# Kernel tuning notes

Measured on AMD Instinct MI355X. Metric: run time of the kernel, lower is better.

Reference implementation:

```python
import jax, jax.numpy as jnp
import numpy as np
from jax import lax

# Fixed Sobel kernels, OIHW layout: [2 out, 1 in, 3, 3]
_GX = np.array([[1, 0, -1], [2, 0, -2], [1, 0, -1]], dtype=np.float32)
_GY = np.array([[1, 2, 1], [0, 0, 0], [-1, -2, -1]], dtype=np.float32)
SOBEL_K = jnp.asarray(np.stack([_GX, _GY], 0)[:, None])  # [2,1,3,3]


def setup_inputs() -> dict:
    key = jax.random.key(0)
    x = jax.random.normal(key, (16, 1, 1024, 1024), dtype=jnp.float32)
    return {"x": x}


def reference(x):
    # Sobel conv, padding=1 (SAME): y [B,2,H,W]
    y = lax.conv_general_dilated(
        x, SOBEL_K, window_strides=(1, 1), padding=((1, 1), (1, 1)),
        dimension_numbers=("NCHW", "OIHW", "NCHW"))
    # sb_x: cross-correlation with [1,-1] along W -> s[:, :-1] - s[:, 1:], then drop last row
    s0 = jnp.sign(y[:, 0:1])                       # [B,1,H,W]
    y0 = (s0[..., :-1] - s0[..., 1:])[..., :-1, :]  # [B,1,H-1,W-1]
    # sb_y: cross-correlation with [1,-1]^T along H -> s[:-1] - s[1:], then drop last col
    s1 = jnp.sign(y[:, 1:2])                       # [B,1,H,W]
    y1 = (s1[..., :-1, :] - s1[..., 1:, :])[..., :-1]  # [B,1,H-1,W-1]
    return (y, y0, y1)
```

## Files before the change

### kernel.cpp

```cpp
#include <hip/hip_runtime.h>


__device__ __forceinline__ void load_raw(const float* __restrict__ xb, int r, int t,
                                         float4& L, float4& C, float4& R) {
    if ((unsigned)r < 1024u) {
        const float4* __restrict__ rp = (const float4*)(xb + (r << 10));
        L = rp[(t > 0) ? (t - 1) : 0];
        C = rp[t];
        R = rp[(t < 255) ? (t + 1) : 255];
    } else {
        L = C = R = make_float4(0.f, 0.f, 0.f, 0.f);
    }
}

__device__ __forceinline__ void cvt_row(float4 L, float4 C, float4 R, int t,
                                        double* __restrict__ o ) {
    float lw = (t > 0)   ? L.w : 0.f;
    float r0 = (t < 255) ? R.x : 0.f;
    float r1 = (t < 255) ? R.y : 0.f;
    o[0] = (double)lw;  o[1] = (double)C.x; o[2] = (double)C.y; o[3] = (double)C.z;
    o[4] = (double)C.w; o[5] = (double)r0;  o[6] = (double)r1;
}

__device__ __forceinline__ float fsign(double v) {
    return (v > 0.0) ? 1.0f : ((v < 0.0) ? -1.0f : 0.0f);
}

__global__ __launch_bounds__(256) void sobel_sign_kernel(const float* __restrict__ x,
                                                         float* __restrict__ out) {
    const int t  = threadIdx.x;
    const int b  = blockIdx.x >> 7;
    const int hg = blockIdx.x & 127;
    const int h0 = hg << 3;
    const int w0 = t << 2;

    const float* __restrict__ xb = x + ((size_t)b << 20);
    float* __restrict__ yb = out + ((size_t)b << 21);
    const size_t NP = (size_t)1023 * 1023;
    float* __restrict__ Y0 = out + 33554432u + (size_t)b * NP;
    float* __restrict__ Y1 = out + 50298896u + (size_t)b * NP;

    __shared__ float s0[1024];
    __shared__ float s1[1024];

    double r[3][7];
    float4 L, C, R;
    load_raw(xb, h0 - 1, t, L, C, R); cvt_row(L, C, R, t, r[0]);
    load_raw(xb, h0,     t, L, C, R); cvt_row(L, C, R, t, r[1]);
    load_raw(xb, h0 + 1, t, L, C, R);

    float psgy[4];

    #pragma unroll
    for (int it = 0; it < 8; ++it) {
        const int h = h0 + it;
        double* A0 = r[it % 3];
        double* A1 = r[(it + 1) % 3];
        double* A2 = r[(it + 2) % 3];
        cvt_row(L, C, R, t, A2);
        load_raw(xb, h + 2, t, L, C, R);

        double tc[7], d[6];
        #pragma unroll
        for (int c = 0; c < 7; ++c) tc[c] = A0[c] + 2.0 * A1[c] + A2[c];
        #pragma unroll
        for (int c = 0; c < 6; ++c) d[c] = A0[c] - A2[c];

        double gx[5], gy[4];
        #pragma unroll
        for (int j = 0; j < 5; ++j) gx[j] = tc[j] - tc[j + 2];
        #pragma unroll
        for (int j = 0; j < 4; ++j) gy[j] = d[j] + 2.0 * d[j + 1] + d[j + 2];

        size_t yo = ((size_t)h << 10) + (size_t)w0;
        *(float4*)(yb + yo) =
            make_float4((float)gx[0], (float)gx[1], (float)gx[2], (float)gx[3]);
        *(float4*)(yb + yo + (1u << 20)) =
            make_float4((float)gy[0], (float)gy[1], (float)gy[2], (float)gy[3]);

        float sgx[5], sgy[4];
        #pragma unroll
        for (int j = 0; j < 5; ++j) sgx[j] = fsign(gx[j]);
        #pragma unroll
        for (int j = 0; j < 4; ++j) sgy[j] = fsign(gy[j]);

        __syncthreads();
        #pragma unroll
        for (int j = 0; j < 4; ++j) {
            s0[w0 + j] = sgx[j] - sgx[j + 1];
            s1[w0 + j] = (it > 0) ? (psgy[j] - sgy[j]) : 0.f;
        }
        __syncthreads();
        #pragma unroll
        for (int k = 0; k < 4; ++k) {
            int c = t + (k << 8);
            bool cok = c < 1023;
            if (h < 1023 && cok) Y0[(size_t)h * 1023u + c] = s0[c];
            if (it > 0 && cok)   Y1[(size_t)(h - 1) * 1023u + c] = s1[c];
        }
        #pragma unroll
        for (int j = 0; j < 4; ++j) psgy[j] = sgy[j];
    }

    {
        const int hl = h0 + 7;
        double bn[7];
        cvt_row(L, C, R, t, bn);
        double* B0 = r[2];
        float y1v[4];
        #pragma unroll
        for (int j = 0; j < 4; ++j) {
            double d0 = B0[j]     - bn[j];
            double d1 = B0[j + 1] - bn[j + 1];
            double d2 = B0[j + 2] - bn[j + 2];
            double gyn = d0 + 2.0 * d1 + d2;
            y1v[j] = psgy[j] - fsign(gyn);
        }
        __syncthreads();
        #pragma unroll
        for (int j = 0; j < 4; ++j) s1[w0 + j] = y1v[j];
        __syncthreads();
        if (hl < 1023) {
            #pragma unroll
            for (int k = 0; k < 4; ++k) {
                int c = t + (k << 8);
                if (c < 1023) Y1[(size_t)hl * 1023u + c] = s1[c];
            }
        }
    }
}

extern "C" void kernel_launch(void* const* d_in, const int* in_sizes, int n_in,
                              void* d_out, int out_size, void* d_ws, size_t ws_size,
                              hipStream_t stream) {
    const float* x = (const float*)d_in[0];
    float* out = (float*)d_out;
    dim3 grid(16 * 128), block(256);
    sobel_sign_kernel<<<grid, block, 0, stream>>>(x, out);
}
```

Before: 318.6 us.

## Halve rows per block, batch sign outputs in shared memory, swizzle block order

Each block now handles 4 rows instead of 8, doubling the grid to 4096 blocks. All sign-difference rows are staged in a 4-row shared buffer with float4 writes, and the per-row pair of barriers is replaced by a single barrier before the output stores. Block indices are also remapped across 8 groups, likely to spread work across XCDs. The intent is more parallelism and less synchronisation, at the cost of more halo rows reloaded per output row.

```diff
diff --git a/kernel.cpp b/kernel.cpp
--- a/kernel.cpp
+++ b/kernel.cpp
@@ -29,19 +29,17 @@
 __global__ __launch_bounds__(256) void sobel_sign_kernel(const float* __restrict__ x,
                                                          float* __restrict__ out) {
     const int t  = threadIdx.x;
-    const int b  = blockIdx.x >> 7;
-    const int hg = blockIdx.x & 127;
-    const int h0 = hg << 3;
+    const int lb = (blockIdx.x & 7) * 512 + (blockIdx.x >> 3);
+    const int b  = lb >> 8;
+    const int hg = lb & 255;
+    const int h0 = hg << 2;
     const int w0 = t << 2;
 
     const float* __restrict__ xb = x + ((size_t)b << 20);
     float* __restrict__ yb = out + ((size_t)b << 21);
-    const size_t NP = (size_t)1023 * 1023;
-    float* __restrict__ Y0 = out + 33554432u + (size_t)b * NP;
-    float* __restrict__ Y1 = out + 50298896u + (size_t)b * NP;
 
-    __shared__ float s0[1024];
-    __shared__ float s1[1024];
+    __shared__ float s0[4][1024];
+    __shared__ float s1[4][1024];
 
     double r[3][7];
     float4 L, C, R;
@@ -52,7 +50,7 @@
     float psgy[4];
 
     #pragma unroll
-    for (int it = 0; it < 8; ++it) {
+    for (int it = 0; it < 4; ++it) {
         const int h = h0 + it;
         double* A0 = r[it % 3];
         double* A1 = r[(it + 1) % 3];
@@ -84,47 +82,49 @@
         #pragma unroll
         for (int j = 0; j < 4; ++j) sgy[j] = fsign(gy[j]);
 
-        __syncthreads();
-        #pragma unroll
-        for (int j = 0; j < 4; ++j) {
-            s0[w0 + j] = sgx[j] - sgx[j + 1];
-            s1[w0 + j] = (it > 0) ? (psgy[j] - sgy[j]) : 0.f;
-        }
-        __syncthreads();
-        #pragma unroll
-        for (int k = 0; k < 4; ++k) {
-            int c = t + (k << 8);
-            bool cok = c < 1023;
-            if (h < 1023 && cok) Y0[(size_t)h * 1023u + c] = s0[c];
-            if (it > 0 && cok)   Y1[(size_t)(h - 1) * 1023u + c] = s1[c];
-        }
+        *(float4*)&s0[it][w0] = make_float4(sgx[0] - sgx[1], sgx[1] - sgx[2],
+                                            sgx[2] - sgx[3], sgx[3] - sgx[4]);
+        if (it > 0)
+            *(float4*)&s1[it - 1][w0] = make_float4(psgy[0] - sgy[0], psgy[1] - sgy[1],
+                                                    psgy[2] - sgy[2], psgy[3] - sgy[3]);
         #pragma unroll
         for (int j = 0; j < 4; ++j) psgy[j] = sgy[j];
     }
 
     {
-        const int hl = h0 + 7;
         double bn[7];
         cvt_row(L, C, R, t, bn);
-        double* B0 = r[2];
-        float y1v[4];
+        double* B0 = r[1];
+        float4 v;
+        float* vp = &v.x;
         #pragma unroll
         for (int j = 0; j < 4; ++j) {
             double d0 = B0[j]     - bn[j];
             double d1 = B0[j + 1] - bn[j + 1];
             double d2 = B0[j + 2] - bn[j + 2];
             double gyn = d0 + 2.0 * d1 + d2;
-            y1v[j] = psgy[j] - fsign(gyn);
+            vp[j] = psgy[j] - fsign(gyn);
         }
-        __syncthreads();
-        #pragma unroll
-        for (int j = 0; j < 4; ++j) s1[w0 + j] = y1v[j];
-        __syncthreads();
-        if (hl < 1023) {
+        *(float4*)&s1[3][w0] = v;
+    }
+
+    __syncthreads();
+
+    const size_t NP = (size_t)1023 * 1023;
+    float* __restrict__ Y0 = out + 33554432u + (size_t)b * NP;
+    float* __restrict__ Y1 = out + 50298896u + (size_t)b * NP;
+    #pragma unroll
+    for (int rr = 0; rr < 4; ++rr) {
+        const int hr = h0 + rr;
+        if (hr < 1023) {
+            const size_t rb = (size_t)hr * 1023u;
             #pragma unroll
             for (int k = 0; k < 4; ++k) {
-                int c = t + (k << 8);
-                if (c < 1023) Y1[(size_t)hl * 1023u + c] = s1[c];
+                const int c = t + (k << 8);
+                if (c < 1023) {
+                    Y0[rb + c] = s0[rr][c];
+                    Y1[rb + c] = s1[rr][c];
+                }
             }
         }
     }
@@ -135,6 +135,6 @@
                               hipStream_t stream) {
     const float* x = (const float*)d_in[0];
     float* out = (float*)d_out;
-    dim3 grid(16 * 128), block(256);
+    dim3 grid(16 * 256), block(256);
     sobel_sign_kernel<<<grid, block, 0, stream>>>(x, out);
 }
```

Measured after the change: 328.8 us. 1.03x slower.
